# Kernel tuning notes

Hardware: AMD Instinct MI355X
Metric: run time of the kernel (lower is better)

Reference implementation:

```python
import jax, jax.numpy as jnp
import numpy as np

N, DEG, D, D2, B, NEG = 65536, 16, 64, 128, 1024, 10
EPS = 1e-12  # F.normalize eps


def setup_inputs() -> dict:
    key = jax.random.key(0)
    ks = jax.random.split(key, 9)
    s1 = 1.0 / np.sqrt(2 * D)
    s2 = 1.0 / np.sqrt(2 * D)
    return {
        "feat_data": jax.random.normal(ks[0], (N, D), jnp.float32),
        "adj": jax.random.randint(ks[1], (N, DEG), 0, N),
        "inputs1": jax.random.randint(ks[2], (B,), 0, N),
        "inputs2": jax.random.randint(ks[3], (B,), 0, N),
        "neg": jax.random.randint(ks[4], (NEG,), 0, N),
        "W1": jax.random.uniform(ks[5], (D, 2 * D), jnp.float32, -s1, s1),
        "b1": jax.random.uniform(ks[6], (D,), jnp.float32, -s1, s1),
        "W2": jax.random.uniform(ks[7], (D2, 2 * D), jnp.float32, -s2, s2),
        "b2": jax.random.uniform(ks[8], (D2,), jnp.float32, -s2, s2),
    }


def reference(feat_data, adj, inputs1, inputs2, neg, W1, b1, W2, b2):
    # Hop-1: per-node neighbor feature sum (gather + reduce), concat self, linear1, tanh.
    # Computed for all nodes (superset of the union the original builds; same values).
    sum1 = feat_data[adj].sum(axis=1)                      # [N, D] gather-heavy
    h1 = jnp.tanh(jnp.concatenate([feat_data, sum1], axis=-1) @ W1.T + b1)  # [N, D]

    def emb(nodes):
        # Hop-2: sum hop-1 embeddings of neighbors, concat raw self features, linear2.
        sum2 = h1[adj[nodes]].sum(axis=1)                  # [b, D]
        out = jnp.concatenate([feat_data[nodes], sum2], axis=-1) @ W2.T + b2  # [b, D2]
        nrm = jnp.maximum(jnp.linalg.norm(out, axis=1, keepdims=True), EPS)
        return out / nrm

    return emb(inputs1), emb(inputs2), emb(neg)
```

## Files before the change

kernel.cpp:

```cpp
#include <hip/hip_runtime.h>
#include <math.h>

#define NN   65536
#define DEGC 16
#define DD   64
#define DD2  128
#define BB   1024
#define NEGC 10
#define NROWS (2 * BB + NEGC)
#define NEDGE (NROWS * DEGC)

__device__ __forceinline__ float tanh_fast(float x) {
    float t = __expf(2.0f * x);
    return 1.0f - 2.0f * __builtin_amdgcn_rcpf(t + 1.0f);
}

__device__ __forceinline__ int node_of_row(int r, const int* __restrict__ in1,
                                           const int* __restrict__ in2,
                                           const int* __restrict__ neg) {
    return (r < BB) ? in1[r] : (r < 2 * BB ? in2[r - BB] : neg[r - 2 * BB]);
}

__global__ __launch_bounds__(256) void hop1_fused(
    const float* __restrict__ feat, const int* __restrict__ adj,
    const int* __restrict__ in1, const int* __restrict__ in2,
    const int* __restrict__ neg,
    const float* __restrict__ W1, const float* __restrict__ b1,
    float* __restrict__ h1) {

    __shared__ float wt[DD2 * 65];
    __shared__ float4 cs4[4][16];

    int tid = threadIdx.x;
    #pragma unroll
    for (int t = 0; t < (DD * DD2) / 256; ++t) {
        int lin = t * 256 + tid;
        int j = lin >> 7, i = lin & 127;
        wt[i * 65 + j] = W1[lin];
    }
    __syncthreads();

    int lane = tid & 63;
    int w = tid >> 6;
    float wreg[DD2];
    #pragma unroll
    for (int i = 0; i < DD2; ++i)
        wreg[i] = wt[i * 65 + lane];
    float bias = b1[lane];

    int wid = blockIdx.x * 4 + w;
    int nw = gridDim.x * 4;
    float* csrow = (float*)&cs4[w][0];

    for (int e0 = wid; e0 < NEDGE; e0 += nw) {
        int e = __builtin_amdgcn_readfirstlane(e0);
        int r = e >> 4, k = e & 15;
        int node = __builtin_amdgcn_readfirstlane(node_of_row(r, in1, in2, neg));
        int n = __builtin_amdgcn_readfirstlane(adj[node * DEGC + k]);
        const int* arow = adj + n * DEGC;
        float s = 0.f;
        #pragma unroll
        for (int k2 = 0; k2 < DEGC; ++k2)
            s += feat[arow[k2] * DD + lane];
        csrow[lane] = s;

        const float* frow = feat + n * DD;
        float acc = bias;
        #pragma unroll
        for (int i4 = 0; i4 < 16; ++i4) {
            float4 c = *(const float4*)(frow + i4 * 4);
            acc += c.x * wreg[i4 * 4 + 0] + c.y * wreg[i4 * 4 + 1]
                 + c.z * wreg[i4 * 4 + 2] + c.w * wreg[i4 * 4 + 3];
        }
        #pragma unroll
        for (int i4 = 0; i4 < 16; ++i4) {
            float4 c = cs4[w][i4];
            acc += c.x * wreg[DD + i4 * 4 + 0] + c.y * wreg[DD + i4 * 4 + 1]
                 + c.z * wreg[DD + i4 * 4 + 2] + c.w * wreg[DD + i4 * 4 + 3];
        }
        h1[e * DD + lane] = tanh_fast(acc);
    }
}

__global__ __launch_bounds__(256) void hop2_fused(
    const float* __restrict__ feat, const float* __restrict__ h1,
    const int* __restrict__ in1, const int* __restrict__ in2,
    const int* __restrict__ neg,
    const float* __restrict__ W2, const float* __restrict__ b2,
    float* __restrict__ out) {

    __shared__ float4 q2[4096];
    __shared__ float4 cs4[8][16];

    int tid = threadIdx.x;
    {
        int j = tid & 127, g0 = tid >> 7;
        #pragma unroll
        for (int g = 0; g < 16; ++g) {
            int i4 = g0 * 16 + g;
            q2[(i4 << 7) | j] = *(const float4*)(W2 + j * DD2 + (i4 << 2));
        }
    }

    int lane = tid & 63;
    int w = tid >> 6;
    int r0 = blockIdx.x * 8 + w * 2;
    int r1 = r0 + 1;
    bool a0 = r0 < NROWS, a1 = r1 < NROWS;

    #pragma unroll
    for (int m = 0; m < 2; ++m) {
        int r = r0 + m;
        if (r < NROWS) {
            const float* base = h1 + (size_t)r * DEGC * DD;
            float s = 0.f;
            #pragma unroll
            for (int k = 0; k < DEGC; ++k)
                s += base[k * DD + lane];
            ((float*)&cs4[w * 2 + m][0])[lane] = s;
        }
    }
    __syncthreads();

    int node0 = a0 ? node_of_row(r0, in1, in2, neg) : 0;
    int node1 = a1 ? node_of_row(r1, in1, in2, neg) : node0;
    node0 = __builtin_amdgcn_readfirstlane(node0);
    node1 = __builtin_amdgcn_readfirstlane(node1);
    const float* cf0 = feat + node0 * DD;
    const float* cf1 = feat + node1 * DD;

    float A0 = b2[lane], B0 = b2[DD + lane];
    float A1 = A0, B1 = B0;

    #pragma unroll
    for (int i4 = 0; i4 < 16; ++i4) {
        float4 wA = q2[(i4 << 7) | lane];
        float4 wB = q2[(i4 << 7) | (64 + lane)];
        float4 c0 = *(const float4*)(cf0 + (i4 << 2));
        float4 c1 = *(const float4*)(cf1 + (i4 << 2));
        A0 += c0.x * wA.x + c0.y * wA.y + c0.z * wA.z + c0.w * wA.w;
        B0 += c0.x * wB.x + c0.y * wB.y + c0.z * wB.z + c0.w * wB.w;
        A1 += c1.x * wA.x + c1.y * wA.y + c1.z * wA.z + c1.w * wA.w;
        B1 += c1.x * wB.x + c1.y * wB.y + c1.z * wB.z + c1.w * wB.w;
    }
    #pragma unroll
    for (int i4 = 0; i4 < 16; ++i4) {
        float4 wA = q2[((16 + i4) << 7) | lane];
        float4 wB = q2[((16 + i4) << 7) | (64 + lane)];
        float4 c0 = cs4[w * 2 + 0][i4];
        float4 c1 = cs4[w * 2 + 1][i4];
        A0 += c0.x * wA.x + c0.y * wA.y + c0.z * wA.z + c0.w * wA.w;
        B0 += c0.x * wB.x + c0.y * wB.y + c0.z * wB.z + c0.w * wB.w;
        A1 += c1.x * wA.x + c1.y * wA.y + c1.z * wA.z + c1.w * wA.w;
        B1 += c1.x * wB.x + c1.y * wB.y + c1.z * wB.z + c1.w * wB.w;
    }

    if (a0) {
        float ss = A0 * A0 + B0 * B0;
        #pragma unroll
        for (int off = 32; off > 0; off >>= 1) ss += __shfl_xor(ss, off, 64);
        float inv = 1.0f / fmaxf(sqrtf(ss), 1e-12f);
        out[r0 * DD2 + lane]      = A0 * inv;
        out[r0 * DD2 + DD + lane] = B0 * inv;
    }
    if (a1) {
        float ss = A1 * A1 + B1 * B1;
        #pragma unroll
        for (int off = 32; off > 0; off >>= 1) ss += __shfl_xor(ss, off, 64);
        float inv = 1.0f / fmaxf(sqrtf(ss), 1e-12f);
        out[r1 * DD2 + lane]      = A1 * inv;
        out[r1 * DD2 + DD + lane] = B1 * inv;
    }
}

extern "C" void kernel_launch(void* const* d_in, const int* in_sizes, int n_in,
                              void* d_out, int out_size, void* d_ws, size_t ws_size,
                              hipStream_t stream) {
    const float* feat = (const float*)d_in[0];
    const int*   adj  = (const int*)d_in[1];
    const int*   in1  = (const int*)d_in[2];
    const int*   in2  = (const int*)d_in[3];
    const int*   neg  = (const int*)d_in[4];
    const float* W1   = (const float*)d_in[5];
    const float* b1   = (const float*)d_in[6];
    const float* W2   = (const float*)d_in[7];
    const float* b2   = (const float*)d_in[8];
    float* out = (float*)d_out;

    float* h1 = (float*)d_ws;

    hop1_fused<<<768, 256, 0, stream>>>(feat, adj, in1, in2, neg, W1, b1, h1);
    hop2_fused<<<(NROWS + 7) / 8, 256, 0, stream>>>(
        feat, h1, in1, in2, neg, W2, b2, out);
}
```

Before: 52.93 us.

## Precompute edge node list and software-pipeline neighbor gathers in hop1

Adds a small kernel that resolves the two-level index chain (input row to node to neighbor) into a flat per-edge node array. hop1 drops the grid-stride loop and gives each wave a contiguous chunk of edges. Within a chunk it prefetches the next edge's 16 neighbor feature gathers while computing the current edge, and splits the dot products into four partial accumulators. The aim is to hide dependent gather latency, at the cost of an extra launch, more registers and fewer blocks.

```diff
diff --git a/kernel.cpp b/kernel.cpp
--- a/kernel.cpp
+++ b/kernel.cpp
@@ -9,22 +9,29 @@
 #define NEGC 10
 #define NROWS (2 * BB + NEGC)
 #define NEDGE (NROWS * DEGC)
+#define H1BLOCKS 512
+#define H1WAVES  (H1BLOCKS * 4)
+#define CHUNK ((NEDGE + H1WAVES - 1) / H1WAVES)
 
 __device__ __forceinline__ float tanh_fast(float x) {
     float t = __expf(2.0f * x);
     return 1.0f - 2.0f * __builtin_amdgcn_rcpf(t + 1.0f);
 }
 
-__device__ __forceinline__ int node_of_row(int r, const int* __restrict__ in1,
-                                           const int* __restrict__ in2,
-                                           const int* __restrict__ neg) {
-    return (r < BB) ? in1[r] : (r < 2 * BB ? in2[r - BB] : neg[r - 2 * BB]);
+__global__ __launch_bounds__(256) void edges_kernel(
+    const int* __restrict__ adj,
+    const int* __restrict__ in1, const int* __restrict__ in2,
+    const int* __restrict__ neg, int* __restrict__ nodes_e) {
+    int e = blockIdx.x * 256 + threadIdx.x;
+    if (e >= NEDGE) return;
+    int r = e >> 4, k = e & 15;
+    int node = (r < BB) ? in1[r] : (r < 2 * BB ? in2[r - BB] : neg[r - 2 * BB]);
+    nodes_e[e] = adj[node * DEGC + k];
 }
 
 __global__ __launch_bounds__(256) void hop1_fused(
     const float* __restrict__ feat, const int* __restrict__ adj,
-    const int* __restrict__ in1, const int* __restrict__ in2,
-    const int* __restrict__ neg,
+    const int* __restrict__ nodes_e,
     const float* __restrict__ W1, const float* __restrict__ b1,
     float* __restrict__ h1) {
 
@@ -49,36 +56,84 @@
     float bias = b1[lane];
 
     int wid = blockIdx.x * 4 + w;
-    int nw = gridDim.x * 4;
+    int e0 = wid * CHUNK;
+    int e1 = min(e0 + CHUNK, NEDGE);
+    if (e0 >= e1) return;
+
     float* csrow = (float*)&cs4[w][0];
 
-    for (int e0 = wid; e0 < NEDGE; e0 += nw) {
-        int e = __builtin_amdgcn_readfirstlane(e0);
-        int r = e >> 4, k = e & 15;
-        int node = __builtin_amdgcn_readfirstlane(node_of_row(r, in1, in2, neg));
-        int n = __builtin_amdgcn_readfirstlane(adj[node * DEGC + k]);
-        const int* arow = adj + n * DEGC;
-        float s = 0.f;
+    int n_cur = __builtin_amdgcn_readfirstlane(nodes_e[e0]);
+    float g[DEGC];
+    {
+        const int* arow = adj + n_cur * DEGC;
         #pragma unroll
         for (int k2 = 0; k2 < DEGC; ++k2)
-            s += feat[arow[k2] * DD + lane];
+            g[k2] = feat[arow[k2] * DD + lane];
+    }
+
+    for (int e = e0; e < e1; ++e) {
+        int enx = (e + 1 < e1) ? e + 1 : e;
+        int n_nxt = __builtin_amdgcn_readfirstlane(nodes_e[enx]);
+
+        const float* frow = feat + (size_t)n_cur * DD;
+        float4 f[16];
+        #pragma unroll
+        for (int i4 = 0; i4 < 16; ++i4)
+            f[i4] = *(const float4*)(frow + i4 * 4);
+
+        float s;
+        {
+            float p[8];
+            #pragma unroll
+            for (int k2 = 0; k2 < 8; ++k2) p[k2] = g[2 * k2] + g[2 * k2 + 1];
+            float q0 = (p[0] + p[1]) + (p[2] + p[3]);
+            float q1 = (p[4] + p[5]) + (p[6] + p[7]);
+            s = q0 + q1;
+        }
         csrow[lane] = s;
 
-        const float* frow = feat + n * DD;
-        float acc = bias;
-        #pragma unroll
-        for (int i4 = 0; i4 < 16; ++i4) {
-            float4 c = *(const float4*)(frow + i4 * 4);
-            acc += c.x * wreg[i4 * 4 + 0] + c.y * wreg[i4 * 4 + 1]
-                 + c.z * wreg[i4 * 4 + 2] + c.w * wreg[i4 * 4 + 3];
-        }
-        #pragma unroll
-        for (int i4 = 0; i4 < 16; ++i4) {
-            float4 c = cs4[w][i4];
-            acc += c.x * wreg[DD + i4 * 4 + 0] + c.y * wreg[DD + i4 * 4 + 1]
-                 + c.z * wreg[DD + i4 * 4 + 2] + c.w * wreg[DD + i4 * 4 + 3];
-        }
-        h1[e * DD + lane] = tanh_fast(acc);
+        float g2[DEGC];
+        {
+            const int* arow2 = adj + n_nxt * DEGC;
+            #pragma unroll
+            for (int k2 = 0; k2 < DEGC; ++k2)
+                g2[k2] = feat[arow2[k2] * DD + lane];
+        }
+
+        float a0 = bias, a1 = 0.f, a2 = 0.f, a3 = 0.f;
+        #pragma unroll
+        for (int i4 = 0; i4 < 16; i4 += 4) {
+            float4 c0 = cs4[w][i4 + 0];
+            float4 c1 = cs4[w][i4 + 1];
+            float4 c2 = cs4[w][i4 + 2];
+            float4 c3 = cs4[w][i4 + 3];
+            a0 += c0.x * wreg[DD + (i4 + 0) * 4 + 0] + c0.y * wreg[DD + (i4 + 0) * 4 + 1]
+                + c0.z * wreg[DD + (i4 + 0) * 4 + 2] + c0.w * wreg[DD + (i4 + 0) * 4 + 3];
+            a1 += c1.x * wreg[DD + (i4 + 1) * 4 + 0] + c1.y * wreg[DD + (i4 + 1) * 4 + 1]
+                + c1.z * wreg[DD + (i4 + 1) * 4 + 2] + c1.w * wreg[DD + (i4 + 1) * 4 + 3];
+            a2 += c2.x * wreg[DD + (i4 + 2) * 4 + 0] + c2.y * wreg[DD + (i4 + 2) * 4 + 1]
+                + c2.z * wreg[DD + (i4 + 2) * 4 + 2] + c2.w * wreg[DD + (i4 + 2) * 4 + 3];
+            a3 += c3.x * wreg[DD + (i4 + 3) * 4 + 0] + c3.y * wreg[DD + (i4 + 3) * 4 + 1]
+                + c3.z * wreg[DD + (i4 + 3) * 4 + 2] + c3.w * wreg[DD + (i4 + 3) * 4 + 3];
+        }
+        #pragma unroll
+        for (int i4 = 0; i4 < 16; i4 += 4) {
+            float4 c0 = f[i4 + 0], c1 = f[i4 + 1], c2 = f[i4 + 2], c3 = f[i4 + 3];
+            a0 += c0.x * wreg[(i4 + 0) * 4 + 0] + c0.y * wreg[(i4 + 0) * 4 + 1]
+                + c0.z * wreg[(i4 + 0) * 4 + 2] + c0.w * wreg[(i4 + 0) * 4 + 3];
+            a1 += c1.x * wreg[(i4 + 1) * 4 + 0] + c1.y * wreg[(i4 + 1) * 4 + 1]
+                + c1.z * wreg[(i4 + 1) * 4 + 2] + c1.w * wreg[(i4 + 1) * 4 + 3];
+            a2 += c2.x * wreg[(i4 + 2) * 4 + 0] + c2.y * wreg[(i4 + 2) * 4 + 1]
+                + c2.z * wreg[(i4 + 2) * 4 + 2] + c2.w * wreg[(i4 + 2) * 4 + 3];
+            a3 += c3.x * wreg[(i4 + 3) * 4 + 0] + c3.y * wreg[(i4 + 3) * 4 + 1]
+                + c3.z * wreg[(i4 + 3) * 4 + 2] + c3.w * wreg[(i4 + 3) * 4 + 3];
+        }
+        float acc = (a0 + a1) + (a2 + a3);
+        h1[(size_t)e * DD + lane] = tanh_fast(acc);
+
+        #pragma unroll
+        for (int k2 = 0; k2 < DEGC; ++k2) g[k2] = g2[k2];
+        n_cur = n_nxt;
     }
 }
 
@@ -122,8 +177,8 @@
     }
     __syncthreads();
 
-    int node0 = a0 ? node_of_row(r0, in1, in2, neg) : 0;
-    int node1 = a1 ? node_of_row(r1, in1, in2, neg) : node0;
+    int node0 = a0 ? ((r0 < BB) ? in1[r0] : (r0 < 2 * BB ? in2[r0 - BB] : neg[r0 - 2 * BB])) : 0;
+    int node1 = a1 ? ((r1 < BB) ? in1[r1] : (r1 < 2 * BB ? in2[r1 - BB] : neg[r1 - 2 * BB])) : node0;
     node0 = __builtin_amdgcn_readfirstlane(node0);
     node1 = __builtin_amdgcn_readfirstlane(node1);
     const float* cf0 = feat + node0 * DD;
@@ -187,9 +242,11 @@
     const float* b2   = (const float*)d_in[8];
     float* out = (float*)d_out;
 
-    float* h1 = (float*)d_ws;
-
-    hop1_fused<<<768, 256, 0, stream>>>(feat, adj, in1, in2, neg, W1, b1, h1);
+    float* h1      = (float*)d_ws;
+    int*   nodes_e = (int*)((char*)d_ws + (size_t)NEDGE * DD * sizeof(float));
+
+    edges_kernel<<<(NEDGE + 255) / 256, 256, 0, stream>>>(adj, in1, in2, neg, nodes_e);
+    hop1_fused<<<H1BLOCKS, 256, 0, stream>>>(feat, adj, nodes_e, W1, b1, h1);
     hop2_fused<<<(NROWS + 7) / 8, 256, 0, stream>>>(
         feat, h1, in1, in2, neg, W2, b2, out);
 }
```

Result: slower. 58.67 us (+10.8%).

## Restructure hop1 to one block per row with batched gathers and LDS weights

Applied to the files above, without the earlier changes.

The grid-stride hop1 loop becomes one block per output row, with each wave handling four edges. The 16 neighbour gathers per edge are issued as independent loads and summed in a tree, and the partial sums go to the global workspace instead of LDS. The matvec then reads W1 from LDS rather than a 128-register array, processing four edges at once. This cuts register pressure and increases memory-level parallelism, at the cost of each of the many more blocks reloading the transposed W1 into LDS and an extra global round trip for the neighbour sums.

```diff
diff --git a/kernel.cpp b/kernel.cpp
--- a/kernel.cpp
+++ b/kernel.cpp
@@ -15,21 +15,14 @@
     return 1.0f - 2.0f * __builtin_amdgcn_rcpf(t + 1.0f);
 }
 
-__device__ __forceinline__ int node_of_row(int r, const int* __restrict__ in1,
-                                           const int* __restrict__ in2,
-                                           const int* __restrict__ neg) {
-    return (r < BB) ? in1[r] : (r < 2 * BB ? in2[r - BB] : neg[r - 2 * BB]);
-}
-
 __global__ __launch_bounds__(256) void hop1_fused(
     const float* __restrict__ feat, const int* __restrict__ adj,
     const int* __restrict__ in1, const int* __restrict__ in2,
     const int* __restrict__ neg,
     const float* __restrict__ W1, const float* __restrict__ b1,
-    float* __restrict__ h1) {
+    float* __restrict__ buf) {
 
     __shared__ float wt[DD2 * 65];
-    __shared__ float4 cs4[4][16];
 
     int tid = threadIdx.x;
     #pragma unroll
@@ -38,48 +31,83 @@
         int j = lin >> 7, i = lin & 127;
         wt[i * 65 + j] = W1[lin];
     }
-    __syncthreads();
 
     int lane = tid & 63;
     int w = tid >> 6;
-    float wreg[DD2];
-    #pragma unroll
-    for (int i = 0; i < DD2; ++i)
-        wreg[i] = wt[i * 65 + lane];
+    int r = blockIdx.x;
+    int node = (r < BB) ? in1[r] : (r < 2 * BB ? in2[r - BB] : neg[r - 2 * BB]);
+    node = __builtin_amdgcn_readfirstlane(node);
+
+    int n[4];
+    #pragma unroll
+    for (int m = 0; m < 4; ++m)
+        n[m] = __builtin_amdgcn_readfirstlane(adj[node * DEGC + w * 4 + m]);
+
+    int ebase = r * DEGC + w * 4;
+
+    #pragma unroll
+    for (int m = 0; m < 4; ++m) {
+        const int* arow = adj + n[m] * DEGC;
+        float g[DEGC];
+        #pragma unroll
+        for (int k2 = 0; k2 < DEGC; ++k2)
+            g[k2] = feat[arow[k2] * DD + lane];
+        float p0 = (g[0] + g[1]) + (g[2] + g[3]);
+        float p1 = (g[4] + g[5]) + (g[6] + g[7]);
+        float p2 = (g[8] + g[9]) + (g[10] + g[11]);
+        float p3 = (g[12] + g[13]) + (g[14] + g[15]);
+        buf[(size_t)(ebase + m) * DD + lane] = (p0 + p1) + (p2 + p3);
+    }
+
+    __syncthreads();
+
     float bias = b1[lane];
-
-    int wid = blockIdx.x * 4 + w;
-    int nw = gridDim.x * 4;
-    float* csrow = (float*)&cs4[w][0];
-
-    for (int e0 = wid; e0 < NEDGE; e0 += nw) {
-        int e = __builtin_amdgcn_readfirstlane(e0);
-        int r = e >> 4, k = e & 15;
-        int node = __builtin_amdgcn_readfirstlane(node_of_row(r, in1, in2, neg));
-        int n = __builtin_amdgcn_readfirstlane(adj[node * DEGC + k]);
-        const int* arow = adj + n * DEGC;
-        float s = 0.f;
-        #pragma unroll
-        for (int k2 = 0; k2 < DEGC; ++k2)
-            s += feat[arow[k2] * DD + lane];
-        csrow[lane] = s;
-
-        const float* frow = feat + n * DD;
-        float acc = bias;
-        #pragma unroll
-        for (int i4 = 0; i4 < 16; ++i4) {
-            float4 c = *(const float4*)(frow + i4 * 4);
-            acc += c.x * wreg[i4 * 4 + 0] + c.y * wreg[i4 * 4 + 1]
-                 + c.z * wreg[i4 * 4 + 2] + c.w * wreg[i4 * 4 + 3];
-        }
-        #pragma unroll
-        for (int i4 = 0; i4 < 16; ++i4) {
-            float4 c = cs4[w][i4];
-            acc += c.x * wreg[DD + i4 * 4 + 0] + c.y * wreg[DD + i4 * 4 + 1]
-                 + c.z * wreg[DD + i4 * 4 + 2] + c.w * wreg[DD + i4 * 4 + 3];
-        }
-        h1[e * DD + lane] = tanh_fast(acc);
-    }
+    float a0 = bias, a1 = bias, a2 = bias, a3 = bias;
+
+    const float* f0 = feat + (size_t)n[0] * DD;
+    const float* f1 = feat + (size_t)n[1] * DD;
+    const float* f2 = feat + (size_t)n[2] * DD;
+    const float* f3 = feat + (size_t)n[3] * DD;
+
+    #pragma unroll
+    for (int i4 = 0; i4 < 16; ++i4) {
+        float w0 = wt[(i4 * 4 + 0) * 65 + lane];
+        float w1v = wt[(i4 * 4 + 1) * 65 + lane];
+        float w2v = wt[(i4 * 4 + 2) * 65 + lane];
+        float w3v = wt[(i4 * 4 + 3) * 65 + lane];
+        float4 c0 = *(const float4*)(f0 + i4 * 4);
+        float4 c1 = *(const float4*)(f1 + i4 * 4);
+        float4 c2 = *(const float4*)(f2 + i4 * 4);
+        float4 c3 = *(const float4*)(f3 + i4 * 4);
+        a0 += c0.x * w0 + c0.y * w1v + c0.z * w2v + c0.w * w3v;
+        a1 += c1.x * w0 + c1.y * w1v + c1.z * w2v + c1.w * w3v;
+        a2 += c2.x * w0 + c2.y * w1v + c2.z * w2v + c2.w * w3v;
+        a3 += c3.x * w0 + c3.y * w1v + c3.z * w2v + c3.w * w3v;
+    }
+    const float* s0 = buf + (size_t)(ebase + 0) * DD;
+    const float* s1 = buf + (size_t)(ebase + 1) * DD;
+    const float* s2 = buf + (size_t)(ebase + 2) * DD;
+    const float* s3 = buf + (size_t)(ebase + 3) * DD;
+    #pragma unroll
+    for (int i4 = 0; i4 < 16; ++i4) {
+        float w0 = wt[(DD + i4 * 4 + 0) * 65 + lane];
+        float w1v = wt[(DD + i4 * 4 + 1) * 65 + lane];
+        float w2v = wt[(DD + i4 * 4 + 2) * 65 + lane];
+        float w3v = wt[(DD + i4 * 4 + 3) * 65 + lane];
+        float4 c0 = *(const float4*)(s0 + i4 * 4);
+        float4 c1 = *(const float4*)(s1 + i4 * 4);
+        float4 c2 = *(const float4*)(s2 + i4 * 4);
+        float4 c3 = *(const float4*)(s3 + i4 * 4);
+        a0 += c0.x * w0 + c0.y * w1v + c0.z * w2v + c0.w * w3v;
+        a1 += c1.x * w0 + c1.y * w1v + c1.z * w2v + c1.w * w3v;
+        a2 += c2.x * w0 + c2.y * w1v + c2.z * w2v + c2.w * w3v;
+        a3 += c3.x * w0 + c3.y * w1v + c3.z * w2v + c3.w * w3v;
+    }
+
+    buf[(size_t)(ebase + 0) * DD + lane] = tanh_fast(a0);
+    buf[(size_t)(ebase + 1) * DD + lane] = tanh_fast(a1);
+    buf[(size_t)(ebase + 2) * DD + lane] = tanh_fast(a2);
+    buf[(size_t)(ebase + 3) * DD + lane] = tanh_fast(a3);
 }
 
 __global__ __launch_bounds__(256) void hop2_fused(
@@ -122,8 +150,8 @@
     }
     __syncthreads();
 
-    int node0 = a0 ? node_of_row(r0, in1, in2, neg) : 0;
-    int node1 = a1 ? node_of_row(r1, in1, in2, neg) : node0;
+    int node0 = a0 ? ((r0 < BB) ? in1[r0] : (r0 < 2 * BB ? in2[r0 - BB] : neg[r0 - 2 * BB])) : 0;
+    int node1 = a1 ? ((r1 < BB) ? in1[r1] : (r1 < 2 * BB ? in2[r1 - BB] : neg[r1 - 2 * BB])) : node0;
     node0 = __builtin_amdgcn_readfirstlane(node0);
     node1 = __builtin_amdgcn_readfirstlane(node1);
     const float* cf0 = feat + node0 * DD;
@@ -187,9 +215,9 @@
     const float* b2   = (const float*)d_in[8];
     float* out = (float*)d_out;
 
-    float* h1 = (float*)d_ws;
-
-    hop1_fused<<<768, 256, 0, stream>>>(feat, adj, in1, in2, neg, W1, b1, h1);
+    float* buf = (float*)d_ws;
+
+    hop1_fused<<<NROWS, 256, 0, stream>>>(feat, adj, in1, in2, neg, W1, b1, buf);
     hop2_fused<<<(NROWS + 7) / 8, 256, 0, stream>>>(
-        feat, h1, in1, in2, neg, W2, b2, out);
-}
+        feat, buf, in1, in2, neg, W2, b2, out);
+}
```

Measured after the change: 62.25 us. +17.6%, slower.
